# Kernel tuning notes

Hardware: AMD Instinct MI355X
Metric: run time of the kernel (lower is better)

Reference implementation:

```python
import math
import jax, jax.numpy as jnp
import numpy as np

B, V, D, H, DE, DFF = 2, 2048, 1024, 16, 256, 4096
DK = D // H


def setup_inputs() -> dict:
    key = jax.random.key(0)
    ks = jax.random.split(key, 24)
    n = lambda k, shape, s=0.02: (jax.random.normal(k, shape, jnp.float32) * s)
    z = lambda *shape: jnp.zeros(shape, jnp.float32)
    return {
        'x': jax.random.normal(ks[0], (B, V, D), jnp.float32),
        'e_node': jax.random.normal(ks[1], (B, V, DE), jnp.float32),
        'conn': jax.random.uniform(ks[2], (B, V, V), jnp.float32),
        'ln1_g': jnp.ones((D,), jnp.float32), 'ln1_b': z(D),
        'f1w1': n(ks[3], (DE, 2 * D)), 'f1b1': z(2 * D),
        'f1w2': n(ks[4], (2 * D, 2 * D)), 'f1b2': z(2 * D),
        'wq': n(ks[5], (D, D)), 'bq': z(D),
        'wk': n(ks[6], (D, D)), 'bk': z(D),
        'wv': n(ks[7], (D, D)), 'bv': z(D),
        'wp': n(ks[8], (D, D)), 'bp': z(D),
        'ln2_g': jnp.ones((D,), jnp.float32), 'ln2_b': z(D),
        'f2w1': n(ks[9], (DE, 2 * D)), 'f2b1': z(2 * D),
        'f2w2': n(ks[10], (2 * D, 2 * D)), 'f2b2': z(2 * D),
        'ffw1': n(ks[11], (D, DFF)), 'ffb1': z(DFF),
        'ffw2': n(ks[12], (DFF, D)), 'ffb2': z(D),
    }


def _ln(x, g, b):
    m = x.mean(-1, keepdims=True)
    v = ((x - m) ** 2).mean(-1, keepdims=True)
    return (x - m) / jnp.sqrt(v + 1e-5) * g + b


def _film(e, w1, b1, w2, b2):
    h = jax.nn.gelu(e @ w1 + b1, approximate=False)  # torch F.gelu default = exact erf
    gb = h @ w2 + b2
    return jnp.split(gb, 2, axis=-1)  # gamma, beta


def reference(x, e_node, conn, ln1_g, ln1_b, f1w1, f1b1, f1w2, f1b2,
              wq, bq, wk, bk, wv, bv, wp, bp, ln2_g, ln2_b,
              f2w1, f2b1, f2w2, f2b2, ffw1, ffb1, ffw2, ffb2):
    b, v, d = x.shape
    # Pre-norm + FiLM 1
    y = _ln(x, ln1_g, ln1_b)
    g1, be1 = _film(e_node, f1w1, f1b1, f1w2, f1b2)
    y = y * (1.0 + g1) + be1
    # Multi-head attention with additive log(conn) mask
    heads = lambda t: t.reshape(b, v, H, DK).transpose(0, 2, 1, 3)  # [B,h,V,dk]
    Q = heads(y @ wq + bq)
    K = heads(y @ wk + bk)
    Vv = heads(y @ wv + bv)
    logits = jnp.einsum('bhqd,bhkd->bhqk', Q, K) / math.sqrt(DK)
    log_mask = jnp.log(jnp.clip(conn, 0.0, 1.0) + 1e-6)[:, None]  # [B,1,V,V]
    s = logits + log_mask
    s = s - s.max(-1, keepdims=True)
    a = jnp.exp(s)
    a = a / (a.sum(-1, keepdims=True) + 1e-8)
    o = jnp.einsum('bhqk,bhkd->bhqd', a, Vv)
    o = o.transpose(0, 2, 1, 3).reshape(b, v, d)
    x = x + (o @ wp + bp)
    # Pre-norm + FiLM 2 + FFN
    y2 = _ln(x, ln2_g, ln2_b)
    g2, be2 = _film(e_node, f2w1, f2b1, f2w2, f2b2)
    y2 = y2 * (1.0 + g2) + be2
    y2 = jax.nn.gelu(y2 @ ffw1 + ffb1, approximate=False) @ ffw2 + ffb2
    return x + y2
```

## Files before the change

kernel.cpp:

```cpp
#include <hip/hip_runtime.h>
#include <math.h>
#include <stdint.h>

#define B_   2
#define V_   2048
#define D_   1024
#define H_   16
#define DK_  64
#define DE_  256
#define DFF_ 4096
#define M_   (B_*V_)
#define D2_  (2*D_)
#define D3_  (3*D_)

typedef unsigned short u16;
typedef unsigned int   u32;
typedef __bf16 bf16x8 __attribute__((ext_vector_type(8)));
typedef u16    u16x8  __attribute__((ext_vector_type(8)));
typedef u16    u16x4  __attribute__((ext_vector_type(4)));
typedef float  f32x4  __attribute__((ext_vector_type(4)));
typedef u32    u32x2  __attribute__((ext_vector_type(2)));
typedef u32    u32x4  __attribute__((ext_vector_type(4)));

__device__ __forceinline__ float bf2f(u16 u) {
    union { unsigned int i; float f; } z; z.i = ((unsigned int)u) << 16; return z.f;
}
__device__ __forceinline__ u16 f2bf(float f) {
    union { float f; unsigned int i; } z; z.f = f;
    unsigned int x = z.i;
    return (u16)((x + 0x7fffu + ((x >> 16) & 1u)) >> 16);
}
__device__ __forceinline__ float gelu_erf(float v) {
    return 0.5f * v * (1.0f + erff(v * 0.70710678118654752f));
}
__device__ __forceinline__ float ldv(const float* p) { return *p; }
__device__ __forceinline__ float ldv(const u16* p)   { return bf2f(*p); }
__device__ __forceinline__ void  stv(float* p, float v) { *p = v; }
__device__ __forceinline__ void  stv(u16* p,   float v) { *p = f2bf(v); }

__device__ __forceinline__ void gload16(const u16* g, u16* lds)
{
    __builtin_amdgcn_global_load_lds(
        (const __attribute__((address_space(1))) void*)g,
        (__attribute__((address_space(3))) void*)(uintptr_t)lds,
        16, 0, 0);
}

__global__ void convT_k(const float* __restrict__ W, u16* __restrict__ Wt, int K, int N)
{
    __shared__ float tile[32][33];
    const int n0 = blockIdx.x * 32, k0 = blockIdx.y * 32;
    const int tx = threadIdx.x, ty = threadIdx.y;
    #pragma unroll
    for (int j = 0; j < 4; ++j)
        tile[ty * 4 + j][tx] = W[(size_t)(k0 + ty * 4 + j) * N + n0 + tx];
    __syncthreads();
    #pragma unroll
    for (int j = 0; j < 4; ++j)
        Wt[(size_t)(n0 + ty * 4 + j) * K + k0 + tx] = f2bf(tile[tx][ty * 4 + j]);
}

__global__ void conv_k(const float* __restrict__ X, u16* __restrict__ Y)
{
    const int i = (blockIdx.x * 256 + threadIdx.x) * 4;
    f32x4 v = *reinterpret_cast<const f32x4*>(X + i);
    u16x4 o;
    #pragma unroll
    for (int j = 0; j < 4; ++j) o[j] = f2bf(v[j]);
    *reinterpret_cast<u16x4*>(Y + i) = o;
}

__global__ void lmask_k(const float* __restrict__ conn, u16* __restrict__ Lm)
{
    const size_t i = ((size_t)blockIdx.x * 256 + threadIdx.x) * 8;
    f32x4 a = *reinterpret_cast<const f32x4*>(conn + i);
    f32x4 b = *reinterpret_cast<const f32x4*>(conn + i + 4);
    u16x8 o;
    #pragma unroll
    for (int j = 0; j < 4; ++j) {
        o[j]     = f2bf(__log2f(fminf(fmaxf(a[j], 0.f), 1.f) + 1e-6f));
        o[j + 4] = f2bf(__log2f(fminf(fmaxf(b[j], 0.f), 1.f) + 1e-6f));
    }
    *reinterpret_cast<u16x8*>(Lm + i) = o;
}

__global__ void qkvbias_k(const float* __restrict__ bq, const float* __restrict__ bk,
                          const float* __restrict__ bv, float* __restrict__ o)
{
    int i = blockIdx.x * 256 + threadIdx.x;
    o[i] = i < 1024 ? bq[i] : (i < 2048 ? bk[i - 1024] : bv[i - 2048]);
}

template<int EPI, int BN, typename TC, typename TRES>
__launch_bounds__(256)
__global__ void gemm_k(const u16* __restrict__ A, const u16* __restrict__ Wt,
                       const float* __restrict__ bias, const TRES* __restrict__ res,
                       TC* __restrict__ C, int M, int N, int K)
{
    constexpr int NB = BN / 32;
    constexpr int IB = BN / 32;
    __shared__ u16 As[128 * 64];
    __shared__ u16 Bs[BN * 64];

    const int tid  = threadIdx.x;
    const int lane = tid & 63;
    const int w    = tid >> 6;
    const int wm   = (w >> 1) * 64, wn = (w & 1) * (BN / 2);
    const int m0   = blockIdx.y * 128, n0 = blockIdx.x * BN;
    const int l15  = lane & 15, l4 = lane >> 4;
    const int rStage = lane >> 3;

    int rrA[4], ccA[4];
    #pragma unroll
    for (int i = 0; i < 4; ++i) {
        rrA[i] = w * 32 + i * 8 + rStage;
        ccA[i] = (lane & 7) ^ (rrA[i] & 7);
    }
    int rrB[IB], ccB[IB];
    #pragma unroll
    for (int i = 0; i < IB; ++i) {
        rrB[i] = w * (BN / 4) + i * 8 + rStage;
        ccB[i] = (lane & 7) ^ (rrB[i] & 7);
    }

    f32x4 acc[4][NB] = {};

    for (int k0 = 0; k0 < K; k0 += 64) {
        if (k0) __syncthreads();
        #pragma unroll
        for (int i = 0; i < 4; ++i)
            gload16(A + (size_t)(m0 + rrA[i]) * K + k0 + ccA[i] * 8, &As[w * 2048 + i * 512]);
        #pragma unroll
        for (int i = 0; i < IB; ++i)
            gload16(Wt + (size_t)(n0 + rrB[i]) * K + k0 + ccB[i] * 8, &Bs[w * (BN * 16) + i * 512]);
        __syncthreads();

        #pragma unroll
        for (int kk = 0; kk < 2; ++kk) {
            bf16x8 a[4], b[NB];
            #pragma unroll
            for (int mb = 0; mb < 4; ++mb) {
                int r  = wm + mb * 16 + l15;
                int ph = (kk * 4 + l4) ^ (r & 7);
                a[mb] = *reinterpret_cast<const bf16x8*>(&As[r * 64 + ph * 8]);
            }
            #pragma unroll
            for (int nb = 0; nb < NB; ++nb) {
                int r  = wn + nb * 16 + l15;
                int ph = (kk * 4 + l4) ^ (r & 7);
                b[nb] = *reinterpret_cast<const bf16x8*>(&Bs[r * 64 + ph * 8]);
            }
            #pragma unroll
            for (int mb = 0; mb < 4; ++mb)
                #pragma unroll
                for (int nb = 0; nb < NB; ++nb)
                    acc[mb][nb] = __builtin_amdgcn_mfma_f32_16x16x32_bf16(a[mb], b[nb], acc[mb][nb], 0, 0, 0);
        }
    }

    #pragma unroll
    for (int nb = 0; nb < NB; ++nb) {
        int col = n0 + wn + nb * 16 + l15;
        float bv = bias[col];
        #pragma unroll
        for (int mb = 0; mb < 4; ++mb) {
            #pragma unroll
            for (int i = 0; i < 4; ++i) {
                int row = m0 + wm + mb * 16 + l4 * 4 + i;
                float v = acc[mb][nb][i] + bv;
                if (EPI == 1) v = gelu_erf(v);
                if (EPI == 2) v += ldv(res + (size_t)row * N + col);
                stv(C + (size_t)row * N + col, v);
            }
        }
    }
}

template<typename TX>
__launch_bounds__(256)
__global__ void lnfilm_k(const TX* __restrict__ X, const u16* __restrict__ GB,
                         const float* __restrict__ g, const float* __restrict__ bb,
                         u16* __restrict__ Y)
{
    const int row = blockIdx.x;
    const int tid = threadIdx.x;
    const int d0  = tid * 4;
    const TX* xr = X + (size_t)row * D_ + d0;
    float xs[4], s = 0.f, sq = 0.f;
    if constexpr (sizeof(TX) == 4) {
        f32x4 v4 = *reinterpret_cast<const f32x4*>(xr);
        #pragma unroll
        for (int j = 0; j < 4; ++j) { xs[j] = v4[j]; s += xs[j]; sq += xs[j] * xs[j]; }
    } else {
        u16x4 v4 = *reinterpret_cast<const u16x4*>(xr);
        #pragma unroll
        for (int j = 0; j < 4; ++j) { xs[j] = bf2f(v4[j]); s += xs[j]; sq += xs[j] * xs[j]; }
    }
    #pragma unroll
    for (int off = 32; off; off >>= 1) {
        s  += __shfl_xor(s, off);
        sq += __shfl_xor(sq, off);
    }
    __shared__ float rs[4], rq[4];
    const int w = tid >> 6;
    if ((tid & 63) == 0) { rs[w] = s; rq[w] = sq; }
    __syncthreads();
    s  = rs[0] + rs[1] + rs[2] + rs[3];
    sq = rq[0] + rq[1] + rq[2] + rq[3];
    const float mean = s * (1.0f / D_);
    const float var  = sq * (1.0f / D_) - mean * mean;
    const float rstd = rsqrtf(fmaxf(var, 0.f) + 1e-5f);
    const u16* gbr = GB + (size_t)row * D2_ + d0;
    u16x4 g4 = *reinterpret_cast<const u16x4*>(gbr);
    u16x4 b4 = *reinterpret_cast<const u16x4*>(gbr + D_);
    f32x4 gg = *reinterpret_cast<const f32x4*>(g + d0);
    f32x4 bv = *reinterpret_cast<const f32x4*>(bb + d0);
    u16x4 o;
    #pragma unroll
    for (int j = 0; j < 4; ++j) {
        float v = (xs[j] - mean) * rstd * gg[j] + bv[j];
        v = v * (1.0f + bf2f(g4[j])) + bf2f(b4[j]);
        o[j] = f2bf(v);
    }
    *reinterpret_cast<u16x4*>(Y + (size_t)row * D_ + d0) = o;
}

__launch_bounds__(256)
__global__ void attn_k(const u16* __restrict__ Q, const u16* __restrict__ K,
                       const u16* __restrict__ Vv, const u16* __restrict__ Lm,
                       u16* __restrict__ O, int ld)
{
    __shared__ u16 Ks[64 * 64];
    __shared__ u16 Vs[64 * 64];
    __shared__ u16 Lms[128 * 64];
    __shared__ u16 Ps[128 * 72];

    const int blk = blockIdx.x;
    const int qt  = blk & 15;
    const int h   = (blk >> 4) & 15;
    const int b   = blk >> 8;
    const int q0  = qt * 128;
    const int tid = threadIdx.x, lane = tid & 63, w = tid >> 6;
    const int l15 = lane & 15, l4 = lane >> 4;
    const size_t bV = (size_t)b * V_;

    bf16x8 qa[2][2];
    #pragma unroll
    for (int g = 0; g < 2; ++g) {
        const u16* qp = Q + (bV + q0 + w * 32 + g * 16 + l15) * ld + h * 64;
        u16x8 r0 = *reinterpret_cast<const u16x8*>(qp + l4 * 8);
        u16x8 r1 = *reinterpret_cast<const u16x8*>(qp + 32 + l4 * 8);
        u16x8 s0, s1;
        #pragma unroll
        for (int j = 0; j < 8; ++j) {
            s0[j] = f2bf(bf2f(r0[j]) * 0.125f);
            s1[j] = f2bf(bf2f(r1[j]) * 0.125f);
        }
        union { u16x8 u; bf16x8 h; } c0, c1;
        c0.u = s0; c1.u = s1;
        qa[g][0] = c0.h; qa[g][1] = c1.h;
    }

    const int rStage = (lane >> 3);
    const int cSw    = ((lane & 7) ^ rStage) * 8;
    const int vK     = ((lane >> 5) << 2) + ((lane & 7) >> 1);
    const int vDk    = ((lane >> 3) & 3) * 16 + (lane & 1) * 8;
    const u32 vaddr  = (u32)(uintptr_t)&Vs[0] + (l4 << 10) + (l15 << 3);

    int lmOff[4];
    #pragma unroll
    for (int kb = 0; kb < 4; ++kb)
        lmOff[kb] = ((((kb << 1) | (l4 >> 1)) ^ (l15 & 7)) << 3);

    const float LOG2E = 1.44269504088896f;
    float lrp[2] = {0.f, 0.f};
    f32x4 o4[2][4] = {};

    for (int kt = 0; kt < V_ / 64; ++kt) {
        const int k0 = kt * 64;
        if (kt) __syncthreads();
        #pragma unroll
        for (int i = 0; i < 2; ++i) {
            int r  = i * 32 + w * 8 + rStage;
            int kv = i * 32 + w * 8 + vK;
            gload16(K  + (bV + k0 + r)  * ld + h * 64 + cSw, &Ks[i * 2048 + w * 512]);
            gload16(Vv + (bV + k0 + kv) * ld + h * 64 + vDk, &Vs[i * 2048 + w * 512]);
        }
        #pragma unroll
        for (int i = 0; i < 4; ++i) {
            int r = i * 32 + w * 8 + rStage;
            gload16(Lm + (bV + q0 + r) * (size_t)V_ + k0 + cSw, &Lms[i * 2048 + w * 512]);
        }
        __syncthreads();

        #pragma unroll
        for (int g = 0; g < 2; ++g) {
            f32x4 s[4];
            #pragma unroll
            for (int kb = 0; kb < 4; ++kb) {
                int row = (kb * 16 + l15) * 64;
                bf16x8 k0f = *reinterpret_cast<const bf16x8*>(&Ks[row + ((l4 ^ (l15 & 7)) * 8)]);
                bf16x8 k1f = *reinterpret_cast<const bf16x8*>(&Ks[row + (((l4 + 4) ^ (l15 & 7)) * 8)]);
                f32x4 z = {};
                z = __builtin_amdgcn_mfma_f32_16x16x32_bf16(k0f, qa[g][0], z, 0, 0, 0);
                z = __builtin_amdgcn_mfma_f32_16x16x32_bf16(k1f, qa[g][1], z, 0, 0, 0);
                s[kb] = z;
            }
            const int lmRow = w * 32 + g * 16 + l15;
            const u16* lmBase = &Lms[lmRow * 64 + (l4 & 1) * 4];
            u16* psW = &Ps[lmRow * 72 + l4 * 4];
            #pragma unroll
            for (int kb = 0; kb < 4; ++kb) {
                u16x4 lm4 = *reinterpret_cast<const u16x4*>(lmBase + lmOff[kb]);
                float p0, p1, p2, p3;
                float t0 = fmaf(s[kb][0], LOG2E, bf2f(lm4[0]));
                float t1 = fmaf(s[kb][1], LOG2E, bf2f(lm4[1]));
                float t2 = fmaf(s[kb][2], LOG2E, bf2f(lm4[2]));
                float t3 = fmaf(s[kb][3], LOG2E, bf2f(lm4[3]));
                asm("v_exp_f32 %0, %1" : "=v"(p0) : "v"(t0));
                asm("v_exp_f32 %0, %1" : "=v"(p1) : "v"(t1));
                asm("v_exp_f32 %0, %1" : "=v"(p2) : "v"(t2));
                asm("v_exp_f32 %0, %1" : "=v"(p3) : "v"(t3));
                lrp[g] += (p0 + p1) + (p2 + p3);
                u32 d0, d1;
                asm("v_cvt_pk_bf16_f32 %0, %1, %2" : "=v"(d0) : "v"(p0), "v"(p1));
                asm("v_cvt_pk_bf16_f32 %0, %1, %2" : "=v"(d1) : "v"(p2), "v"(p3));
                u32x2 dd = {d0, d1};
                *reinterpret_cast<u32x2*>(psW + kb * 16) = dd;
            }
        }

        union VU { u32x4 u; bf16x8 h; };
        VU vb[2][4];
        #pragma unroll
        for (int c2 = 0; c2 < 2; ++c2) {
            u32 a0 = vaddr + c2 * 4096;
            u32x2 t0, t1, t2, t3, t4, t5, t6, t7;
            asm volatile("ds_read_b64_tr_b16 %0, %1"            : "=v"(t0) : "v"(a0));
            asm volatile("ds_read_b64_tr_b16 %0, %1 offset:512" : "=v"(t1) : "v"(a0));
            asm volatile("ds_read_b64_tr_b16 %0, %1 offset:128" : "=v"(t2) : "v"(a0));
            asm volatile("ds_read_b64_tr_b16 %0, %1 offset:640" : "=v"(t3) : "v"(a0));
            asm volatile("ds_read_b64_tr_b16 %0, %1 offset:256" : "=v"(t4) : "v"(a0));
            asm volatile("ds_read_b64_tr_b16 %0, %1 offset:768" : "=v"(t5) : "v"(a0));
            asm volatile("ds_read_b64_tr_b16 %0, %1 offset:384" : "=v"(t6) : "v"(a0));
            asm volatile("ds_read_b64_tr_b16 %0, %1 offset:896" : "=v"(t7) : "v"(a0));
            asm volatile("s_waitcnt lgkmcnt(0)" ::: "memory");
            __builtin_amdgcn_sched_barrier(0);
            vb[c2][0].u = (u32x4){t0.x, t0.y, t1.x, t1.y};
            vb[c2][1].u = (u32x4){t2.x, t2.y, t3.x, t3.y};
            vb[c2][2].u = (u32x4){t4.x, t4.y, t5.x, t5.y};
            vb[c2][3].u = (u32x4){t6.x, t6.y, t7.x, t7.y};
        }
        #pragma unroll
        for (int g = 0; g < 2; ++g) {
            const u16* pr = &Ps[(w * 32 + g * 16 + l15) * 72];
            bf16x8 pa0 = *reinterpret_cast<const bf16x8*>(pr + l4 * 8);
            bf16x8 pa1 = *reinterpret_cast<const bf16x8*>(pr + 32 + l4 * 8);
            #pragma unroll
            for (int nb = 0; nb < 4; ++nb) {
                o4[g][nb] = __builtin_amdgcn_mfma_f32_16x16x32_bf16(pa0, vb[0][nb].h, o4[g][nb], 0, 0, 0);
                o4[g][nb] = __builtin_amdgcn_mfma_f32_16x16x32_bf16(pa1, vb[1][nb].h, o4[g][nb], 0, 0, 0);
            }
        }
    }

    #pragma unroll
    for (int g = 0; g < 2; ++g) {
        float v = lrp[g];
        v += __shfl_xor(v, 16);
        v += __shfl_xor(v, 32);
        #pragma unroll
        for (int i = 0; i < 4; ++i) {
            float lw = __shfl(v, (lane & 48) | ((l4 << 2) + i));
            float rcp = 1.0f / (lw + 1e-8f);
            int q = q0 + w * 32 + g * 16 + l4 * 4 + i;
            u16* op = O + (bV + q) * D_ + h * 64;
            #pragma unroll
            for (int nb = 0; nb < 4; ++nb)
                op[nb * 16 + l15] = f2bf(o4[g][nb][i] * rcp);
        }
    }
}

extern "C" void kernel_launch(void* const* d_in, const int* in_sizes, int n_in,
                              void* d_out, int out_size, void* d_ws, size_t ws_size,
                              hipStream_t stream)
{
    (void)in_sizes; (void)n_in; (void)out_size; (void)ws_size;
    const float* x    = (const float*)d_in[0];
    const float* e    = (const float*)d_in[1];
    const float* conn = (const float*)d_in[2];
    const float* ln1g = (const float*)d_in[3];
    const float* ln1b = (const float*)d_in[4];
    const float* f1w1 = (const float*)d_in[5];
    const float* f1b1 = (const float*)d_in[6];
    const float* f1w2 = (const float*)d_in[7];
    const float* f1b2 = (const float*)d_in[8];
    const float* wq   = (const float*)d_in[9];
    const float* bq   = (const float*)d_in[10];
    const float* wk   = (const float*)d_in[11];
    const float* bk   = (const float*)d_in[12];
    const float* wv   = (const float*)d_in[13];
    const float* bv   = (const float*)d_in[14];
    const float* wp   = (const float*)d_in[15];
    const float* bp   = (const float*)d_in[16];
    const float* ln2g = (const float*)d_in[17];
    const float* ln2b = (const float*)d_in[18];
    const float* f2w1 = (const float*)d_in[19];
    const float* f2b1 = (const float*)d_in[20];
    const float* f2w2 = (const float*)d_in[21];
    const float* f2b2 = (const float*)d_in[22];
    const float* ffw1 = (const float*)d_in[23];
    const float* ffb1 = (const float*)d_in[24];
    const float* ffw2 = (const float*)d_in[25];
    const float* ffb2 = (const float*)d_in[26];
    float* out = (float*)d_out;

    char* ws = (char*)d_ws;
    const size_t MB = 1u << 20;
    u16*   Lm    = (u16*)(ws + 0);
    u16*   e_bf  = (u16*)(ws + 16 * MB);
    u16*   h     = (u16*)(ws + 18 * MB);
    u16*   wt2   = (u16*)(ws + 34 * MB);
    u16*   wt8   = (u16*)(ws + 36 * MB);
    u16*   gb    = (u16*)(ws + 44 * MB);
    u16*   y     = (u16*)(ws + 60 * MB);
    u16*   wqkvt = (u16*)(ws + 18 * MB);
    u16*   qkv   = (u16*)(ws + 24 * MB);
    float* qkvb  = (float*)(ws + 71 * MB);
    u16*   o     = (u16*)(ws + 48 * MB);
    u16*   xnew  = (u16*)(ws + 64 * MB);
    u16*   h2    = (u16*)(ws + 18 * MB);
    u16*   gb2   = (u16*)(ws + 44 * MB);
    u16*   y2    = (u16*)(ws + 0);
    u16*   ffw1t = (u16*)(ws + 8 * MB);
    u16*   t     = (u16*)(ws + 16 * MB);
    u16*   ffw2t = (u16*)(ws + 48 * MB);

    dim3 blk(256), tblk(32, 8);
    #define CONVT(W, WT, K, N) convT_k<<<dim3((N)/32, (K)/32), tblk, 0, stream>>>(W, WT, K, N)

    conv_k <<<(M_*DE_)/1024, blk, 0, stream>>>(e, e_bf);
    lmask_k<<<(B_*(size_t)V_*V_)/2048, blk, 0, stream>>>(conn, Lm);

    CONVT(f1w1, wt2, DE_, D2_);
    gemm_k<1, 64, u16, u16><<<dim3(D2_/64, M_/128), blk, 0, stream>>>(e_bf, wt2, f1b1, (const u16*)nullptr, h, M_, D2_, DE_);
    CONVT(f1w2, wt8, D2_, D2_);
    gemm_k<0, 64, u16, u16><<<dim3(D2_/64, M_/128), blk, 0, stream>>>(h, wt8, f1b2, (const u16*)nullptr, gb, M_, D2_, D2_);
    lnfilm_k<float><<<M_, blk, 0, stream>>>(x, gb, ln1g, ln1b, y);
    CONVT(wq, wqkvt,                 D_, D_);
    CONVT(wk, wqkvt + 1024 * 1024,   D_, D_);
    CONVT(wv, wqkvt + 2048 * 1024,   D_, D_);
    qkvbias_k<<<D3_/256, blk, 0, stream>>>(bq, bk, bv, qkvb);
    gemm_k<0, 128, u16, u16><<<dim3(D3_/128, M_/128), blk, 0, stream>>>(y, wqkvt, qkvb, (const u16*)nullptr, qkv, M_, D3_, D_);
    attn_k<<<B_*H_*(V_/128), blk, 0, stream>>>(qkv, qkv + 1024, qkv + 2048, Lm, o, D3_);
    CONVT(wp, wt2, D_, D_);
    gemm_k<2, 64, u16, float><<<dim3(D_/64, M_/128), blk, 0, stream>>>(o, wt2, bp, x, xnew, M_, D_, D_);
    CONVT(f2w1, wt2, DE_, D2_);
    gemm_k<1, 64, u16, u16><<<dim3(D2_/64, M_/128), blk, 0, stream>>>(e_bf, wt2, f2b1, (const u16*)nullptr, h2, M_, D2_, DE_);
    CONVT(f2w2, wt8, D2_, D2_);
    gemm_k<0, 64, u16, u16><<<dim3(D2_/64, M_/128), blk, 0, stream>>>(h2, wt8, f2b2, (const u16*)nullptr, gb2, M_, D2_, D2_);
    lnfilm_k<u16><<<M_, blk, 0, stream>>>(xnew, gb2, ln2g, ln2b, y2);
    CONVT(ffw1, ffw1t, D_, DFF_);
    gemm_k<1, 128, u16, u16><<<dim3(DFF_/128, M_/128), blk, 0, stream>>>(y2, ffw1t, ffb1, (const u16*)nullptr, t, M_, DFF_, D_);
    CONVT(ffw2, ffw2t, DFF_, D_);
    gemm_k<2, 64, float, u16><<<dim3(D_/64, M_/128), blk, 0, stream>>>(t, ffw2t, ffb2, xnew, out, M_, D_, DFF_);
    #undef CONVT
}
```

Baseline: 413.7 us.

## Add 256x256 double-buffered GEMM for QKV and FFN1, raise MFMA priority

Adds a 512-thread GEMM kernel with 256x256 output tiles. It uses double-buffered LDS tiles with an XOR swizzle, and each wave computes a 128x64 sub-tile in four phases. The QKV projection and the first FFN layer now use it, to get more operand reuse per global load than the 128-wide tile kernel. It also wraps the MFMA sections in the attention kernel and the new GEMM with s_setprio to favour matrix issue. The cost is fewer blocks: QKV launches only 192 blocks on the GPU. The 128KB of LDS per block also limits each CU to a single block.

```diff
diff --git a/kernel.cpp b/kernel.cpp
--- a/kernel.cpp
+++ b/kernel.cpp
@@ -170,6 +170,103 @@
                 float v = acc[mb][nb][i] + bv;
                 if (EPI == 1) v = gelu_erf(v);
                 if (EPI == 2) v += ldv(res + (size_t)row * N + col);
+                stv(C + (size_t)row * N + col, v);
+            }
+        }
+    }
+}
+
+template<int EPI, typename TC>
+__launch_bounds__(512, 2)
+__global__ void gemm256_k(const u16* __restrict__ A, const u16* __restrict__ Wt,
+                          const float* __restrict__ bias,
+                          TC* __restrict__ C, int M, int N, int K)
+{
+    __shared__ u16 As[2][256 * 64];
+    __shared__ u16 Bs[2][256 * 64];
+
+    const int tid  = threadIdx.x;
+    const int lane = tid & 63;
+    const int w    = tid >> 6;
+    const int wm   = (w >> 2) * 128;
+    const int wn   = (w & 3) * 64;
+    const int m0   = blockIdx.y * 256, n0 = blockIdx.x * 256;
+    const int l15  = lane & 15, l4 = lane >> 4;
+
+    int rr[4], cc[4];
+    #pragma unroll
+    for (int i = 0; i < 4; ++i) {
+        rr[i] = i * 64 + w * 8 + (lane >> 3);
+        cc[i] = (lane & 7) ^ (rr[i] & 7);
+    }
+
+    f32x4 acc[8][4] = {};
+    const int NT = K / 64;
+
+    #pragma unroll
+    for (int i = 0; i < 4; ++i) {
+        gload16(A  + (size_t)(m0 + rr[i]) * K + cc[i] * 8, &As[0][i * 4096 + w * 512]);
+        gload16(Wt + (size_t)(n0 + rr[i]) * K + cc[i] * 8, &Bs[0][i * 4096 + w * 512]);
+    }
+
+    for (int t = 0; t < NT; ++t) {
+        const int d = t & 1;
+        __syncthreads();
+
+        if (t + 1 < NT) {
+            const int k1 = (t + 1) * 64;
+            #pragma unroll
+            for (int i = 0; i < 4; ++i) {
+                gload16(A  + (size_t)(m0 + rr[i]) * K + k1 + cc[i] * 8, &As[d ^ 1][i * 4096 + w * 512]);
+                gload16(Wt + (size_t)(n0 + rr[i]) * K + k1 + cc[i] * 8, &Bs[d ^ 1][i * 4096 + w * 512]);
+            }
+        }
+
+        #pragma unroll
+        for (int ph = 0; ph < 4; ++ph) {
+            const int mh = ph >> 1, nh = ph & 1;
+            bf16x8 a[4][2], b[2][2];
+            #pragma unroll
+            for (int mf = 0; mf < 4; ++mf)
+                #pragma unroll
+                for (int kk = 0; kk < 2; ++kk) {
+                    int r  = wm + (mh * 4 + mf) * 16 + l15;
+                    int p2 = (kk * 4 + l4) ^ (r & 7);
+                    a[mf][kk] = *reinterpret_cast<const bf16x8*>(&As[d][r * 64 + p2 * 8]);
+                }
+            #pragma unroll
+            for (int nf = 0; nf < 2; ++nf)
+                #pragma unroll
+                for (int kk = 0; kk < 2; ++kk) {
+                    int r  = wn + (nh * 2 + nf) * 16 + l15;
+                    int p2 = (kk * 4 + l4) ^ (r & 7);
+                    b[nf][kk] = *reinterpret_cast<const bf16x8*>(&Bs[d][r * 64 + p2 * 8]);
+                }
+            __builtin_amdgcn_s_setprio(1);
+            #pragma unroll
+            for (int mf = 0; mf < 4; ++mf)
+                #pragma unroll
+                for (int nf = 0; nf < 2; ++nf)
+                    #pragma unroll
+                    for (int kk = 0; kk < 2; ++kk)
+                        acc[mh * 4 + mf][nh * 2 + nf] = __builtin_amdgcn_mfma_f32_16x16x32_bf16(
+                            a[mf][kk], b[nf][kk], acc[mh * 4 + mf][nh * 2 + nf], 0, 0, 0);
+            __builtin_amdgcn_s_setprio(0);
+            __builtin_amdgcn_sched_barrier(0);
+        }
+    }
+
+    #pragma unroll
+    for (int nf = 0; nf < 4; ++nf) {
+        int col = n0 + wn + nf * 16 + l15;
+        float bv = bias[col];
+        #pragma unroll
+        for (int mf = 0; mf < 8; ++mf) {
+            #pragma unroll
+            for (int i = 0; i < 4; ++i) {
+                int row = m0 + wm + mf * 16 + l4 * 4 + i;
+                float v = acc[mf][nf][i] + bv;
+                if (EPI == 1) v = gelu_erf(v);
                 stv(C + (size_t)row * N + col, v);
             }
         }
@@ -302,8 +399,10 @@
                 bf16x8 k0f = *reinterpret_cast<const bf16x8*>(&Ks[row + ((l4 ^ (l15 & 7)) * 8)]);
                 bf16x8 k1f = *reinterpret_cast<const bf16x8*>(&Ks[row + (((l4 + 4) ^ (l15 & 7)) * 8)]);
                 f32x4 z = {};
+                __builtin_amdgcn_s_setprio(1);
                 z = __builtin_amdgcn_mfma_f32_16x16x32_bf16(k0f, qa[g][0], z, 0, 0, 0);
                 z = __builtin_amdgcn_mfma_f32_16x16x32_bf16(k1f, qa[g][1], z, 0, 0, 0);
+                __builtin_amdgcn_s_setprio(0);
                 s[kb] = z;
             }
             const int lmRow = w * 32 + g * 16 + l15;
@@ -356,11 +455,13 @@
             const u16* pr = &Ps[(w * 32 + g * 16 + l15) * 72];
             bf16x8 pa0 = *reinterpret_cast<const bf16x8*>(pr + l4 * 8);
             bf16x8 pa1 = *reinterpret_cast<const bf16x8*>(pr + 32 + l4 * 8);
+            __builtin_amdgcn_s_setprio(1);
             #pragma unroll
             for (int nb = 0; nb < 4; ++nb) {
                 o4[g][nb] = __builtin_amdgcn_mfma_f32_16x16x32_bf16(pa0, vb[0][nb].h, o4[g][nb], 0, 0, 0);
                 o4[g][nb] = __builtin_amdgcn_mfma_f32_16x16x32_bf16(pa1, vb[1][nb].h, o4[g][nb], 0, 0, 0);
             }
+            __builtin_amdgcn_s_setprio(0);
         }
     }
 
@@ -437,7 +538,7 @@
     u16*   t     = (u16*)(ws + 16 * MB);
     u16*   ffw2t = (u16*)(ws + 48 * MB);
 
-    dim3 blk(256), tblk(32, 8);
+    dim3 blk(256), blk512(512), tblk(32, 8);
     #define CONVT(W, WT, K, N) convT_k<<<dim3((N)/32, (K)/32), tblk, 0, stream>>>(W, WT, K, N)
 
     conv_k <<<(M_*DE_)/1024, blk, 0, stream>>>(e, e_bf);
@@ -452,7 +553,7 @@
     CONVT(wk, wqkvt + 1024 * 1024,   D_, D_);
     CONVT(wv, wqkvt + 2048 * 1024,   D_, D_);
     qkvbias_k<<<D3_/256, blk, 0, stream>>>(bq, bk, bv, qkvb);
-    gemm_k<0, 128, u16, u16><<<dim3(D3_/128, M_/128), blk, 0, stream>>>(y, wqkvt, qkvb, (const u16*)nullptr, qkv, M_, D3_, D_);
+    gemm256_k<0, u16><<<dim3(D3_/256, M_/256), blk512, 0, stream>>>(y, wqkvt, qkvb, qkv, M_, D3_, D_);
     attn_k<<<B_*H_*(V_/128), blk, 0, stream>>>(qkv, qkv + 1024, qkv + 2048, Lm, o, D3_);
     CONVT(wp, wt2, D_, D_);
     gemm_k<2, 64, u16, float><<<dim3(D_/64, M_/128), blk, 0, stream>>>(o, wt2, bp, x, xnew, M_, D_, D_);
@@ -462,7 +563,7 @@
     gemm_k<0, 64, u16, u16><<<dim3(D2_/64, M_/128), blk, 0, stream>>>(h2, wt8, f2b2, (const u16*)nullptr, gb2, M_, D2_, D2_);
     lnfilm_k<u16><<<M_, blk, 0, stream>>>(xnew, gb2, ln2g, ln2b, y2);
     CONVT(ffw1, ffw1t, D_, DFF_);
-    gemm_k<1, 128, u16, u16><<<dim3(DFF_/128, M_/128), blk, 0, stream>>>(y2, ffw1t, ffb1, (const u16*)nullptr, t, M_, DFF_, D_);
+    gemm256_k<1, u16><<<dim3(DFF_/256, M_/256), blk512, 0, stream>>>(y2, ffw1t, ffb1, t, M_, DFF_, D_);
     CONVT(ffw2, ffw2t, DFF_, D_);
     gemm_k<2, 64, float, u16><<<dim3(D_/64, M_/128), blk, 0, stream>>>(t, ffw2t, ffb2, xnew, out, M_, D_, DFF_);
     #undef CONVT
```

Measured after the change: 417.5 us. No clear change (+0.9%).

## Double-buffer GEMM LDS tiles to overlap global loads with MFMA

Applied to the files above, without the earlier changes.

The GEMM kernel now keeps two LDS buffers for the A and B tiles and issues the global-to-LDS loads for the next K tile before computing on the current one. Partial vmcnt waits let the current tile's loads finish while the next tile's loads stay in flight, hiding global memory latency behind the MFMA work. In exchange, LDS use per block doubles, which may reduce occupancy. Correctness also depends on the hand-coded vmcnt counts matching the number of load instructions issued.

```diff
diff --git a/kernel.cpp b/kernel.cpp
--- a/kernel.cpp
+++ b/kernel.cpp
@@ -46,6 +46,13 @@
         16, 0, 0);
 }
 
+__device__ __forceinline__ void barrier_raw()
+{
+    asm volatile("" ::: "memory");
+    __builtin_amdgcn_s_barrier();
+    asm volatile("" ::: "memory");
+}
+
 __global__ void convT_k(const float* __restrict__ W, u16* __restrict__ Wt, int K, int N)
 {
     __shared__ float tile[32][33];
@@ -99,8 +106,8 @@
 {
     constexpr int NB = BN / 32;
     constexpr int IB = BN / 32;
-    __shared__ u16 As[128 * 64];
-    __shared__ u16 Bs[BN * 64];
+    __shared__ u16 As[2][128 * 64];
+    __shared__ u16 Bs[2][BN * 64];
 
     const int tid  = threadIdx.x;
     const int lane = tid & 63;
@@ -123,17 +130,33 @@
         ccB[i] = (lane & 7) ^ (rrB[i] & 7);
     }
 
+    auto stage = [&](int kt, int dd) {
+        const int k0 = kt * 64;
+        #pragma unroll
+        for (int i = 0; i < 4; ++i)
+            gload16(A + (size_t)(m0 + rrA[i]) * K + k0 + ccA[i] * 8, &As[dd][w * 2048 + i * 512]);
+        #pragma unroll
+        for (int i = 0; i < IB; ++i)
+            gload16(Wt + (size_t)(n0 + rrB[i]) * K + k0 + ccB[i] * 8, &Bs[dd][w * (BN * 16) + i * 512]);
+    };
+
     f32x4 acc[4][NB] = {};
-
-    for (int k0 = 0; k0 < K; k0 += 64) {
-        if (k0) __syncthreads();
-        #pragma unroll
-        for (int i = 0; i < 4; ++i)
-            gload16(A + (size_t)(m0 + rrA[i]) * K + k0 + ccA[i] * 8, &As[w * 2048 + i * 512]);
-        #pragma unroll
-        for (int i = 0; i < IB; ++i)
-            gload16(Wt + (size_t)(n0 + rrB[i]) * K + k0 + ccB[i] * 8, &Bs[w * (BN * 16) + i * 512]);
-        __syncthreads();
+    const int NT = K / 64;
+
+    stage(0, 0);
+
+    for (int t = 0; t < NT; ++t) {
+        const int d = t & 1;
+        barrier_raw();
+        if (t + 1 < NT) {
+            stage(t + 1, d ^ 1);
+            if constexpr (BN == 128) asm volatile("s_waitcnt vmcnt(8)" ::: "memory");
+            else                     asm volatile("s_waitcnt vmcnt(6)" ::: "memory");
+        } else {
+            asm volatile("s_waitcnt vmcnt(0)" ::: "memory");
+        }
+        barrier_raw();
+        __builtin_amdgcn_sched_barrier(0);
 
         #pragma unroll
         for (int kk = 0; kk < 2; ++kk) {
@@ -142,13 +165,13 @@
             for (int mb = 0; mb < 4; ++mb) {
                 int r  = wm + mb * 16 + l15;
                 int ph = (kk * 4 + l4) ^ (r & 7);
-                a[mb] = *reinterpret_cast<const bf16x8*>(&As[r * 64 + ph * 8]);
+                a[mb] = *reinterpret_cast<const bf16x8*>(&As[d][r * 64 + ph * 8]);
             }
             #pragma unroll
             for (int nb = 0; nb < NB; ++nb) {
                 int r  = wn + nb * 16 + l15;
                 int ph = (kk * 4 + l4) ^ (r & 7);
-                b[nb] = *reinterpret_cast<const bf16x8*>(&Bs[r * 64 + ph * 8]);
+                b[nb] = *reinterpret_cast<const bf16x8*>(&Bs[d][r * 64 + ph * 8]);
             }
             #pragma unroll
             for (int mb = 0; mb < 4; ++mb)
```

New measurement: 402.3 us. 1.03x faster.
